# Performance work log

Hardware: AMD Instinct MI355X
Metric: run time of the kernel (lower is better)

The kernel has to match this reference:

```python
import jax, jax.numpy as jnp
import numpy as np


def unfold_wo_center(x, kernel_size, dilation):
    # x: [N, C, H, W] -> [N, C, K*K-1, H, W]; same semantics as F.unfold with
    # the given dilation/padding, reshaped and with the center tap removed.
    N, C, H, W = x.shape
    pad = (kernel_size + (dilation - 1) * (kernel_size - 1)) // 2
    xp = jnp.pad(x, ((0, 0), (0, 0), (pad, pad), (pad, pad)))
    center = (kernel_size * kernel_size) // 2
    taps = []
    idx = 0
    for i in range(kernel_size):      # row-major kernel order (matches F.unfold)
        for j in range(kernel_size):
            if idx != center:
                taps.append(xp[:, :, i * dilation:i * dilation + H,
                                     j * dilation:j * dilation + W])
            idx += 1
    return jnp.stack(taps, axis=2)


def setup_inputs() -> dict:
    key = jax.random.key(0)
    mask_logits = jax.random.normal(key, (64, 1, 256, 256), dtype=jnp.float32)
    return {"mask_logits": mask_logits, "pairwise_size": 3, "pairwise_dilation": 2}


def reference(mask_logits, pairwise_size, pairwise_dilation):
    # compute_pairwise_term from BoxSeg's DynamicMaskHead
    log_fg = jax.nn.log_sigmoid(mask_logits)    # [N,1,H,W]
    log_bg = jax.nn.log_sigmoid(-mask_logits)
    fg_u = unfold_wo_center(log_fg, pairwise_size, pairwise_dilation)  # [N,1,K2-1,H,W]
    bg_u = unfold_wo_center(log_bg, pairwise_size, pairwise_dilation)
    # stable log(exp(a)+exp(b)) = logaddexp
    log_same = jnp.logaddexp(log_fg[:, :, None] + fg_u,
                             log_bg[:, :, None] + bg_u)
    return -log_same[:, 0]                      # [N, K2-1, H, W]
```

## Files before the change

### kernel.cpp

```cpp
#include <hip/hip_runtime.h>
#include <hip/hip_bf16.h>


#define N_IMG 64
#define H_DIM 256
#define W_DIM 256

__device__ __forceinline__ float log_sig(float x) {
    float t = __expf(-fabsf(x));
    return fminf(x, 0.0f) - __logf(1.0f + t);
}

__global__ __launch_bounds__(256) void pairwise_term_kernel(
        const float* __restrict__ x, float* __restrict__ out) {
    const int idx = blockIdx.x * blockDim.x + threadIdx.x;
    const int total = N_IMG * H_DIM * W_DIM;
    if (idx >= total) return;

    const int w = idx & (W_DIM - 1);
    const int h = (idx >> 8) & (H_DIM - 1);
    const int n = idx >> 16;

    const float xc = x[idx];
    const float lf = log_sig(xc);
    const float lb = lf - xc;

    const int dy[8] = {-2, -2, -2,  0, 0,  2, 2, 2};
    const int dx[8] = {-2,  0,  2, -2, 2, -2, 0, 2};

    float* outp = out + (size_t)n * 8 * H_DIM * W_DIM + h * W_DIM + w;

#pragma unroll
    for (int t = 0; t < 8; ++t) {
        const int hh = h + dy[t];
        const int ww = w + dx[t];
        float lf_t = 0.0f, lb_t = 0.0f;
        if ((unsigned)hh < H_DIM && (unsigned)ww < W_DIM) {
            const float xt = x[idx + dy[t] * W_DIM + dx[t]];
            lf_t = log_sig(xt);
            lb_t = lf_t - xt;
        }
        const float a = lf + lf_t;
        const float b = lb + lb_t;
        const float m = fmaxf(a, b);
        const float r = m + __logf(1.0f + __expf(-fabsf(a - b)));
        outp[(size_t)t * H_DIM * W_DIM] = -r;
    }
}

extern "C" void kernel_launch(void* const* d_in, const int* in_sizes, int n_in,
                              void* d_out, int out_size, void* d_ws, size_t ws_size,
                              hipStream_t stream) {
    const float* x = (const float*)d_in[0];
    float* out = (float*)d_out;
    const int total = N_IMG * H_DIM * W_DIM;
    const int block = 256;
    const int grid = (total + block - 1) / block;
    pairwise_term_kernel<<<grid, block, 0, stream>>>(x, out);
}
```

Before: 178.6 us.

## Vectorize pairwise term four pixels per thread with a closed-form log-sigmoid identity

Each thread now handles four adjacent pixels. It loads its three input rows as vector loads and reuses the log-sigmoid values across all eight taps instead of recomputing them per tap. The logaddexp is replaced with the identity log_sig(a+b) - log_sig(a) - log_sig(b), and out-of-bounds taps are set directly to zero. Outputs are written as 16-byte nontemporal stores. This cuts transcendental work and the number of memory instructions, at the cost of more registers per thread and a quarter as many threads.

```diff
diff --git a/kernel.cpp b/kernel.cpp
--- a/kernel.cpp
+++ b/kernel.cpp
@@ -2,49 +2,74 @@
 #include <hip/hip_bf16.h>
 
 
-#define N_IMG 64
+#define NI 64
 #define H_DIM 256
 #define W_DIM 256
 
-__device__ __forceinline__ float log_sig(float x) {
-    float t = __expf(-fabsf(x));
-    return fminf(x, 0.0f) - __logf(1.0f + t);
+typedef float f32x2 __attribute__((ext_vector_type(2)));
+typedef float f32x4 __attribute__((ext_vector_type(4)));
+
+__device__ __forceinline__ float log_sig(float v) {
+    return fminf(v, 0.0f) - __logf(1.0f + __expf(-fabsf(v)));
 }
 
-__global__ __launch_bounds__(256) void pairwise_term_kernel(
+__global__ __launch_bounds__(256) void pairwise_term_v2(
         const float* __restrict__ x, float* __restrict__ out) {
-    const int idx = blockIdx.x * blockDim.x + threadIdx.x;
-    const int total = N_IMG * H_DIM * W_DIM;
-    if (idx >= total) return;
+    const int tid = blockIdx.x * blockDim.x + threadIdx.x;
+    const int w4 = (tid & 63) << 2;
+    const int h  = (tid >> 6) & (H_DIM - 1);
+    const int n  = tid >> 14;
 
-    const int w = idx & (W_DIM - 1);
-    const int h = (idx >> 8) & (H_DIM - 1);
-    const int n = idx >> 16;
+    const float* img = x + (size_t)n * (H_DIM * W_DIM);
 
-    const float xc = x[idx];
-    const float lf = log_sig(xc);
-    const float lb = lf - xc;
+    float xv[3][8];
+    float lfv[3][8];
+    bool  rowv[3];
 
-    const int dy[8] = {-2, -2, -2,  0, 0,  2, 2, 2};
-    const int dx[8] = {-2,  0,  2, -2, 2, -2, 0, 2};
+#pragma unroll
+    for (int r = 0; r < 3; ++r) {
+        const int hh = h + 2 * (r - 1);
+        rowv[r] = (unsigned)hh < H_DIM;
+        const float* rp = img + (size_t)(rowv[r] ? hh : h) * W_DIM;
+        const int lc = (w4 == 0) ? 0 : w4 - 2;
+        const int rc = (w4 == W_DIM - 4) ? W_DIM - 2 : w4 + 4;
+        const f32x2 a = *reinterpret_cast<const f32x2*>(rp + lc);
+        const f32x4 b = *reinterpret_cast<const f32x4*>(rp + w4);
+        const f32x2 c = *reinterpret_cast<const f32x2*>(rp + rc);
+        xv[r][0] = a.x; xv[r][1] = a.y;
+        xv[r][2] = b.x; xv[r][3] = b.y; xv[r][4] = b.z; xv[r][5] = b.w;
+        xv[r][6] = c.x; xv[r][7] = c.y;
+#pragma unroll
+        for (int cc = 0; cc < 8; ++cc) lfv[r][cc] = log_sig(xv[r][cc]);
+    }
 
-    float* outp = out + (size_t)n * 8 * H_DIM * W_DIM + h * W_DIM + w;
+    bool colv[8];
+#pragma unroll
+    for (int cc = 0; cc < 8; ++cc) {
+        colv[cc] = (unsigned)(w4 - 2 + cc) < W_DIM;
+    }
+
+    const int tr[8]  = {0, 0, 0, 1, 1, 2, 2, 2};
+    const int tco[8] = {0, 2, 4, 0, 4, 0, 2, 4};
+
+    float* op = out + ((size_t)n * 8 * H_DIM + h) * W_DIM + w4;
 
 #pragma unroll
     for (int t = 0; t < 8; ++t) {
-        const int hh = h + dy[t];
-        const int ww = w + dx[t];
-        float lf_t = 0.0f, lb_t = 0.0f;
-        if ((unsigned)hh < H_DIM && (unsigned)ww < W_DIM) {
-            const float xt = x[idx + dy[t] * W_DIM + dx[t]];
-            lf_t = log_sig(xt);
-            lb_t = lf_t - xt;
+        const int r  = tr[t];
+        const int co = tco[t];
+        float res[4];
+#pragma unroll
+        for (int p = 0; p < 4; ++p) {
+            const int ci = p + co;
+            const float s = xv[1][p + 2] + xv[r][ci];
+            const float v = log_sig(s) - lfv[1][p + 2] - lfv[r][ci];
+            res[p] = (rowv[r] && colv[ci]) ? v : 0.0f;
         }
-        const float a = lf + lf_t;
-        const float b = lb + lb_t;
-        const float m = fmaxf(a, b);
-        const float r = m + __logf(1.0f + __expf(-fabsf(a - b)));
-        outp[(size_t)t * H_DIM * W_DIM] = -r;
+        f32x4 vec;
+        vec.x = res[0]; vec.y = res[1]; vec.z = res[2]; vec.w = res[3];
+        __builtin_nontemporal_store(
+            vec, reinterpret_cast<f32x4*>(op + (size_t)t * (H_DIM * W_DIM)));
     }
 }
 
@@ -53,8 +78,8 @@
                               hipStream_t stream) {
     const float* x = (const float*)d_in[0];
     float* out = (float*)d_out;
-    const int total = N_IMG * H_DIM * W_DIM;
+    const int total_threads = NI * H_DIM * W_DIM / 4;
     const int block = 256;
-    const int grid = (total + block - 1) / block;
-    pairwise_term_kernel<<<grid, block, 0, stream>>>(x, out);
+    const int grid = total_threads / block;
+    pairwise_term_v2<<<grid, block, 0, stream>>>(x, out);
 }
```

Measured after the change: 154.6 us. 1.16x faster.
